# Kernel optimization log

Hardware: AMD Instinct MI355X
Metric: run time of the kernel (lower is better)

The kernel has to match this reference:

```python
import jax, jax.numpy as jnp
import numpy as np

NUM_HEADS = 8
KERNEL = 7  # kernel_size (kh == kw == 7), dilation 1, non-causal


def _na_indices(L, k):
    # NATTEN neighborhood: window start clamped so the kxk window stays in-bounds
    starts = jnp.clip(jnp.arange(L) - k // 2, 0, L - k)  # [L]
    return starts[:, None] + jnp.arange(k)               # [L, k]


def setup_inputs() -> dict:
    key = jax.random.key(0)
    k1, k2, k3 = jax.random.split(key, 3)
    B, H, W, C = 1, 64, 128, 256
    x = jax.random.normal(k1, (B, H, W, C), dtype=jnp.float32)
    # weights stored as [in, out] so y = x @ w + b (equivalent to torch Linear math)
    w_qkv = jax.random.normal(k2, (C, 3 * C), dtype=jnp.float32) * 0.02
    b_qkv = jnp.zeros((3 * C,), dtype=jnp.float32)
    w_proj = jax.random.normal(k3, (C, C), dtype=jnp.float32) * 0.02
    b_proj = jnp.zeros((C,), dtype=jnp.float32)
    return {"x": x, "w_qkv": w_qkv, "b_qkv": b_qkv, "w_proj": w_proj, "b_proj": b_proj}


def reference(x, w_qkv, b_qkv, w_proj, b_proj):
    B, H, W, C = x.shape
    nh = NUM_HEADS
    hd = C // nh
    scale = hd ** -0.5
    kk = KERNEL

    qkv = (x @ w_qkv + b_qkv).reshape(B, H, W, 3, nh, hd)
    q = qkv[:, :, :, 0]  # [B,H,W,nh,hd]
    k = qkv[:, :, :, 1]
    v = qkv[:, :, :, 2]

    ih = _na_indices(H, kk)  # [H,kk]
    iw = _na_indices(W, kk)  # [W,kk]

    # gather K/V neighborhoods: [B,H,kh,W,kw,nh,hd]
    k_win = k[:, ih][:, :, :, iw]
    v_win = v[:, ih][:, :, :, iw]

    # scores: query vs its kh*kw neighbors
    attn = jnp.einsum('bhwnd,bhpwqnd->bhwnpq', q * scale, k_win)  # [B,H,W,nh,kh,kw]
    attn = jax.nn.softmax(attn.reshape(B, H, W, nh, kk * kk), axis=-1)
    attn = attn.reshape(B, H, W, nh, kk, kk)

    out = jnp.einsum('bhwnpq,bhpwqnd->bhwnd', attn, v_win)  # [B,H,W,nh,hd]
    out = out.reshape(B, H, W, C)
    return out @ w_proj + b_proj
```

## Files before the change

kernel.cpp:

```cpp
#include <hip/hip_runtime.h>
#include <cmath>

#define HH 64
#define WW 128
#define CC 256
#define NHEAD 8
#define HDIM 32
#define NPIX (HH*WW)
#define QKV_N (3*CC)

#define KSLOT 248
#define LDK   40
#define VSLOT 264

typedef __attribute__((ext_vector_type(8))) short short8v;
typedef __attribute__((ext_vector_type(4))) short short4v;
typedef __attribute__((ext_vector_type(4))) float f32x4;
typedef unsigned int u32;

__device__ __forceinline__ short f2bf(float f) {
    unsigned int u = __builtin_bit_cast(unsigned int, f);
    u += 0x7fffu + ((u >> 16) & 1u);
    return (short)(u >> 16);
}

__global__ __launch_bounds__(256)
void prep_w(const float* __restrict__ w_qkv, const float* __restrict__ w_proj,
            short* __restrict__ wq_t, short* __restrict__ wp_t)
{
    __shared__ float tile[32][33];
    int idx = blockIdx.x;
    const float* src; short* dst; int N;
    if (idx < 192) { src = w_qkv;  dst = wq_t; N = QKV_N; }
    else { idx -= 192; src = w_proj; dst = wp_t; N = CC; }
    const int nbx = N / 32;
    const int bn = (idx % nbx) * 32;
    const int bk = (idx / nbx) * 32;
    const int tx = threadIdx.x & 31, ty = threadIdx.x >> 5;
#pragma unroll
    for (int i = 0; i < 32; i += 8)
        tile[ty + i][tx] = src[(size_t)(bk + ty + i) * N + bn + tx];
    __syncthreads();
#pragma unroll
    for (int i = 0; i < 32; i += 8)
        dst[(size_t)(bn + ty + i) * CC + bk + tx] = f2bf(tile[tx][ty + i]);
}

__global__ __launch_bounds__(256)
void gemm_qkv(const float* __restrict__ A, const short* __restrict__ Bt,
              const float* __restrict__ bias, short* __restrict__ Cp)
{
    __shared__ short As[64 * 40];
    __shared__ short Bs[2][128 * 32];

    const int tid = threadIdx.x, lane = tid & 63, wave = tid >> 6;
    const int wm0 = (wave >> 1) * 32, wn0 = (wave & 1) * 64;
    const int bm = blockIdx.x * 64, bn = blockIdx.y * 128;
    const int l15 = lane & 15, l4 = lane >> 4;
    const int arow = tid >> 2, akoff = (tid & 3) * 8;

    f32x4 acc[2][4];
#pragma unroll
    for (int i = 0; i < 2; ++i)
#pragma unroll
        for (int j = 0; j < 4; ++j) acc[i][j] = (f32x4){0.f, 0.f, 0.f, 0.f};

    auto stageB = [&](int buf, int t) {
#pragma unroll
        for (int i = 0; i < 2; ++i) {
            const int g = tid + 256 * i;
            const int row = g >> 2, gr = g & 3;
            __builtin_amdgcn_global_load_lds(
                (const __attribute__((address_space(1))) u32*)
                    (Bt + (size_t)(bn + row) * CC + t * 32 + ((gr ^ (row & 3)) * 8)),
                (__attribute__((address_space(3))) u32*)&Bs[buf][g * 8], 16, 0, 0);
        }
    };

    float4 a0, a1;
    {
        const float* p = A + (size_t)(bm + arow) * CC + akoff;
        a0 = *(const float4*)p; a1 = *(const float4*)(p + 4);
    }
    stageB(0, 0);

    for (int t = 0; t < 8; ++t) {
        const int cur = t & 1;
        __syncthreads();
        {
            short8v w;
            w[0] = f2bf(a0.x); w[1] = f2bf(a0.y); w[2] = f2bf(a0.z); w[3] = f2bf(a0.w);
            w[4] = f2bf(a1.x); w[5] = f2bf(a1.y); w[6] = f2bf(a1.z); w[7] = f2bf(a1.w);
            *(short8v*)&As[arow * 40 + akoff] = w;
        }
        __syncthreads();
        if (t + 1 < 8) {
            const float* p = A + (size_t)(bm + arow) * CC + (t + 1) * 32 + akoff;
            a0 = *(const float4*)p; a1 = *(const float4*)(p + 4);
            stageB(cur ^ 1, t + 1);
        }

        short8v af[2], bf[4];
#pragma unroll
        for (int fm = 0; fm < 2; ++fm)
            af[fm] = *(const short8v*)&As[(wm0 + fm * 16 + l15) * 40 + l4 * 8];
#pragma unroll
        for (int fn = 0; fn < 4; ++fn) {
            const int row = wn0 + fn * 16 + l15;
            bf[fn] = *(const short8v*)&Bs[cur][row * 32 + ((l4 ^ (row & 3)) * 8)];
        }
#pragma unroll
        for (int fm = 0; fm < 2; ++fm)
#pragma unroll
            for (int fn = 0; fn < 4; ++fn)
                acc[fm][fn] = __builtin_amdgcn_mfma_f32_16x16x32_bf16(
                    af[fm], bf[fn], acc[fm][fn], 0, 0, 0);
    }

    const int col0 = bn + wn0 + l15;
    const int row0 = bm + wm0 + l4 * 4;
#pragma unroll
    for (int fn = 0; fn < 4; ++fn) {
        const int cc = col0 + fn * 16;
        const float bv = bias[cc];
#pragma unroll
        for (int fm = 0; fm < 2; ++fm)
#pragma unroll
            for (int r = 0; r < 4; ++r) {
                const int rr = row0 + fm * 16 + r;
                Cp[((size_t)(cc >> 5) * NPIX + rr) * HDIM + (cc & 31)] =
                    f2bf(acc[fm][fn][r] + bv);
            }
    }
}

__global__ __launch_bounds__(256)
void gemm_proj(const short* __restrict__ A, const short* __restrict__ Bt,
               const float* __restrict__ bias, float* __restrict__ C)
{
    __shared__ short As[2][64 * 32];
    __shared__ short Bs[2][128 * 32];

    const int tid = threadIdx.x, lane = tid & 63, wave = tid >> 6;
    const int wm0 = (wave >> 1) * 32, wn0 = (wave & 1) * 64;
    const int bm = blockIdx.x * 64, bn = blockIdx.y * 128;
    const int l15 = lane & 15, l4 = lane >> 4;

    f32x4 acc[2][4];
#pragma unroll
    for (int i = 0; i < 2; ++i)
#pragma unroll
        for (int j = 0; j < 4; ++j) acc[i][j] = (f32x4){0.f, 0.f, 0.f, 0.f};

    auto stage = [&](int buf, int t) {
        {
            const int row = tid >> 2, gr = tid & 3;
            __builtin_amdgcn_global_load_lds(
                (const __attribute__((address_space(1))) u32*)
                    (A + (size_t)(bm + row) * CC + t * 32 + ((gr ^ (row & 3)) * 8)),
                (__attribute__((address_space(3))) u32*)&As[buf][tid * 8], 16, 0, 0);
        }
#pragma unroll
        for (int i = 0; i < 2; ++i) {
            const int g = tid + 256 * i;
            const int row = g >> 2, gr = g & 3;
            __builtin_amdgcn_global_load_lds(
                (const __attribute__((address_space(1))) u32*)
                    (Bt + (size_t)(bn + row) * CC + t * 32 + ((gr ^ (row & 3)) * 8)),
                (__attribute__((address_space(3))) u32*)&Bs[buf][g * 8], 16, 0, 0);
        }
    };

    stage(0, 0);

    for (int t = 0; t < 8; ++t) {
        const int cur = t & 1;
        __syncthreads();
        if (t + 1 < 8) stage(cur ^ 1, t + 1);

        short8v af[2], bf[4];
#pragma unroll
        for (int fm = 0; fm < 2; ++fm) {
            const int row = wm0 + fm * 16 + l15;
            af[fm] = *(const short8v*)&As[cur][row * 32 + ((l4 ^ (row & 3)) * 8)];
        }
#pragma unroll
        for (int fn = 0; fn < 4; ++fn) {
            const int row = wn0 + fn * 16 + l15;
            bf[fn] = *(const short8v*)&Bs[cur][row * 32 + ((l4 ^ (row & 3)) * 8)];
        }
#pragma unroll
        for (int fm = 0; fm < 2; ++fm)
#pragma unroll
            for (int fn = 0; fn < 4; ++fn)
                acc[fm][fn] = __builtin_amdgcn_mfma_f32_16x16x32_bf16(
                    af[fm], bf[fn], acc[fm][fn], 0, 0, 0);
    }

    const int col0 = bn + wn0 + l15;
    const int row0 = bm + wm0 + l4 * 4;
#pragma unroll
    for (int fn = 0; fn < 4; ++fn) {
        const float bv = bias[col0 + fn * 16];
#pragma unroll
        for (int fm = 0; fm < 2; ++fm)
#pragma unroll
            for (int r = 0; r < 4; ++r)
                C[(size_t)(row0 + fm * 16 + r) * CC + col0 + fn * 16] =
                    acc[fm][fn][r] + bv;
    }
}

__global__ __launch_bounds__(256)
void na_mfma(const short* __restrict__ qkv, short* __restrict__ attn)
{
    __shared__ short Ksh[KSLOT * LDK];
    __shared__ short Vsh[32 * VSLOT];

    const int x0 = blockIdx.x * 16;
    const int y0 = blockIdx.y * 4;
    const int head = blockIdx.z;
    const int tid = threadIdx.x, lane = tid & 63, w = tid >> 6;
    const int rs  = min(max(y0 - 3, 0), HH - 7);
    const int wsx = x0 - 3;
    const short* Qp = qkv + (size_t)head * NPIX * HDIM;
    const short* Kp = qkv + (size_t)(NHEAD + head) * NPIX * HDIM;
    const short* Vp = qkv + (size_t)(2 * NHEAD + head) * NPIX * HDIM;

    for (int idx = tid; idx < 880; idx += 256) {
        int g = idx & 3, rc = idx >> 2;
        int i = rc / 22, c = rc - i * 22;
        int yy = rs + i, xx = wsx + c;
        if (yy < HH && (unsigned)xx < WW)
            *(short8v*)&Ksh[(i * 24 + c) * LDK + g * 8] =
                *(const short8v*)(Kp + (size_t)(yy * WW + xx) * HDIM + g * 8);
    }
    for (int idx = tid; idx < 264; idx += 256) {
        int g = idx & 3, q2 = idx >> 2;
        int i = q2 / 6, cq = q2 - i * 6;
        int yy = rs + i;
        short8v vv[4];
#pragma unroll
        for (int j = 0; j < 4; ++j) {
            int c = cq * 4 + j, xx = wsx + c;
            if (yy < HH && c < 22 && (unsigned)xx < WW)
                vv[j] = *(const short8v*)(Vp + (size_t)(yy * WW + xx) * HDIM + g * 8);
            else {
                short8v z = {0,0,0,0,0,0,0,0};
                vv[j] = z;
            }
        }
#pragma unroll
        for (int jd = 0; jd < 8; ++jd) {
            short4v s4 = {vv[0][jd], vv[1][jd], vv[2][jd], vv[3][jd]};
            *(short4v*)&Vsh[(g * 8 + jd) * VSLOT + i * 24 + cq * 4] = s4;
        }
    }

    const int l15 = lane & 15, l4 = lane >> 4;
    const int y = y0 + w;
    short8v qf = *(const short8v*)(Qp + (size_t)(y * WW + x0 + l15) * HDIM + l4 * 8);
    __syncthreads();

    const int wbase = (min(max(y - 3, 0), HH - 7) - rs) * 24;

    f32x4 sacc[11];
#pragma unroll
    for (int kc = 0; kc < 11; ++kc) {
        short8v kf = *(const short8v*)&Ksh[(wbase + kc * 16 + l15) * LDK + l4 * 8];
        f32x4 z = {0.f, 0.f, 0.f, 0.f};
        sacc[kc] = __builtin_amdgcn_mfma_f32_16x16x32_bf16(kf, qf, z, 0, 0, 0);
    }

    const int xq = x0 + l15;
    const int cw = min(max(xq - 3, 0), WW - 7) - wsx;
    const float scale = 0.17677669529663687f;
    float lsum = 0.f;
#pragma unroll
    for (int kc = 0; kc < 11; ++kc) {
#pragma unroll
        for (int r = 0; r < 4; ++r) {
            int kl = kc * 16 + l4 * 4 + r;
            int row = kl / 24;
            int c = kl - row * 24;
            bool valid = (row < 7) && (c >= cw) && (c <= cw + 6);
            float e = valid ? __expf(sacc[kc][r] * scale) : 0.f;
            sacc[kc][r] = e;
            lsum += e;
        }
    }
    lsum += __shfl_xor(lsum, 16);
    lsum += __shfl_xor(lsum, 32);
    const float inv = 1.0f / lsum;

    short4v pf[12];
#pragma unroll
    for (int kc = 0; kc < 11; ++kc) {
        short4v pk;
#pragma unroll
        for (int r = 0; r < 4; ++r) pk[r] = f2bf(sacc[kc][r] * inv);
        pf[kc] = pk;
    }
    pf[11] = (short4v){0, 0, 0, 0};

    const int src0 = ((l4 & 1) << 5) + l15;
    const int src1 = src0 + 16;
    const bool hi = (l4 & 2) != 0;
    f32x4 oacc[2];
    oacc[0] = (f32x4){0.f, 0.f, 0.f, 0.f};
    oacc[1] = (f32x4){0.f, 0.f, 0.f, 0.f};
#pragma unroll
    for (int kc2 = 0; kc2 < 6; ++kc2) {
        int lo0 = ((const int*)&pf[2 * kc2])[0];
        int lo1 = ((const int*)&pf[2 * kc2])[1];
        int hi0 = ((const int*)&pf[2 * kc2 + 1])[0];
        int hi1 = ((const int*)&pf[2 * kc2 + 1])[1];
        int a0 = __shfl(lo0, src0), a1 = __shfl(lo1, src0);
        int a2 = __shfl(lo0, src1), a3 = __shfl(lo1, src1);
        int b0 = __shfl(hi0, src0), b1 = __shfl(hi1, src0);
        int b2 = __shfl(hi0, src1), b3 = __shfl(hi1, src1);
        int w0 = hi ? b0 : a0, w1 = hi ? b1 : a1;
        int w2 = hi ? b2 : a2, w3 = hi ? b3 : a3;
        int wv[4] = {w0, w1, w2, w3};
        short8v bfrag = *(const short8v*)wv;
#pragma unroll
        for (int nc = 0; nc < 2; ++nc) {
            short8v vf = *(const short8v*)&Vsh[(nc * 16 + l15) * VSLOT
                                               + wbase + kc2 * 32 + l4 * 8];
            oacc[nc] = __builtin_amdgcn_mfma_f32_16x16x32_bf16(vf, bfrag, oacc[nc], 0, 0, 0);
        }
    }

    short* op = attn + (size_t)(y * WW + x0 + l15) * CC + head * HDIM;
#pragma unroll
    for (int nc = 0; nc < 2; ++nc) {
        short4v o;
#pragma unroll
        for (int r = 0; r < 4; ++r) o[r] = f2bf(oacc[nc][r]);
        *(short4v*)(op + nc * 16 + l4 * 4) = o;
    }
}

extern "C" void kernel_launch(void* const* d_in, const int* in_sizes, int n_in,
                              void* d_out, int out_size, void* d_ws, size_t ws_size,
                              hipStream_t stream)
{
    const float* x      = (const float*)d_in[0];
    const float* w_qkv  = (const float*)d_in[1];
    const float* b_qkv  = (const float*)d_in[2];
    const float* w_proj = (const float*)d_in[3];
    const float* b_proj = (const float*)d_in[4];
    float* out = (float*)d_out;

    char* ws = (char*)d_ws;
    short* qkv_r   = (short*)ws;
    short* attn_bf = (short*)(ws + 12582912);
    short* wq_t    = (short*)(ws + 16777216);
    short* wp_t    = (short*)(ws + 17170432);

    prep_w<<<dim3(256), dim3(256), 0, stream>>>(w_qkv, w_proj, wq_t, wp_t);

    gemm_qkv<<<dim3(NPIX / 64, QKV_N / 128), dim3(256), 0, stream>>>(
        x, wq_t, b_qkv, qkv_r);

    na_mfma<<<dim3(WW / 16, HH / 4, NHEAD), dim3(256), 0, stream>>>(qkv_r, attn_bf);

    gemm_proj<<<dim3(NPIX / 64, CC / 128), dim3(256), 0, stream>>>(
        attn_bf, wp_t, b_proj, out);
}
```

Baseline: 43.89 us.

## Fuse four stages into one persistent kernel with hierarchical grid barriers

```diff
diff --git a/kernel.cpp b/kernel.cpp
--- a/kernel.cpp
+++ b/kernel.cpp
@@ -8,6 +8,7 @@
 #define HDIM 32
 #define NPIX (HH*WW)
 #define QKV_N (3*CC)
+#define NBLK 1024u
 
 #define KSLOT 248
 #define LDK   40
@@ -24,12 +25,39 @@
     return (short)(u >> 16);
 }
 
-__global__ __launch_bounds__(256)
-void prep_w(const float* __restrict__ w_qkv, const float* __restrict__ w_proj,
-            short* __restrict__ wq_t, short* __restrict__ wp_t)
-{
-    __shared__ float tile[32][33];
-    int idx = blockIdx.x;
+__device__ __forceinline__ void grid_sync(u32* syncb, u32 bar, int bid)
+{
+    __syncthreads();
+    if (threadIdx.x == 0) {
+        u32* sub   = syncb + (bid & 7) * 32;
+        u32* top   = syncb + 8 * 32;
+        u32* flagv = syncb + (9 + (bid & 7)) * 32;
+        u32 prev = __hip_atomic_fetch_add(sub, 1u, __ATOMIC_ACQ_REL,
+                                          __HIP_MEMORY_SCOPE_AGENT);
+        if (prev == bar * (NBLK / 8u) - 1u) {
+            u32 p2 = __hip_atomic_fetch_add(top, 1u, __ATOMIC_ACQ_REL,
+                                            __HIP_MEMORY_SCOPE_AGENT);
+            if (p2 == bar * 8u - 1u) {
+#pragma unroll
+                for (int r = 0; r < 8; ++r)
+                    __hip_atomic_store(syncb + (9 + r) * 32, bar,
+                                       __ATOMIC_RELEASE, __HIP_MEMORY_SCOPE_AGENT);
+            }
+        }
+        while (__hip_atomic_fetch_add(flagv, 0u, __ATOMIC_RELAXED,
+                                      __HIP_MEMORY_SCOPE_AGENT) < bar)
+            __builtin_amdgcn_s_sleep(32);
+        (void)__hip_atomic_load(flagv, __ATOMIC_ACQUIRE,
+                                __HIP_MEMORY_SCOPE_AGENT);
+    }
+    __syncthreads();
+}
+
+__device__ __forceinline__ void prep_unit(float* ldsf, int idx,
+    const float* __restrict__ w_qkv, const float* __restrict__ w_proj,
+    short* __restrict__ wq_t, short* __restrict__ wp_t)
+{
+    float (*tile)[33] = reinterpret_cast<float(*)[33]>(ldsf);
     const float* src; short* dst; int N;
     if (idx < 192) { src = w_qkv;  dst = wq_t; N = QKV_N; }
     else { idx -= 192; src = w_proj; dst = wp_t; N = CC; }
@@ -46,16 +74,15 @@
         dst[(size_t)(bn + ty + i) * CC + bk + tx] = f2bf(tile[tx][ty + i]);
 }
 
-__global__ __launch_bounds__(256)
-void gemm_qkv(const float* __restrict__ A, const short* __restrict__ Bt,
-              const float* __restrict__ bias, short* __restrict__ Cp)
-{
-    __shared__ short As[64 * 40];
-    __shared__ short Bs[2][128 * 32];
+__device__ __forceinline__ void qkv_tile(short* lds,
+    const float* __restrict__ A, const short* __restrict__ Bt,
+    const float* __restrict__ bias, short* __restrict__ Cp, int bm, int bn)
+{
+    short* As = lds;
+    short* Bs = lds + 64 * 40;
 
     const int tid = threadIdx.x, lane = tid & 63, wave = tid >> 6;
     const int wm0 = (wave >> 1) * 32, wn0 = (wave & 1) * 64;
-    const int bm = blockIdx.x * 64, bn = blockIdx.y * 128;
     const int l15 = lane & 15, l4 = lane >> 4;
     const int arow = tid >> 2, akoff = (tid & 3) * 8;
 
@@ -73,7 +100,8 @@
             __builtin_amdgcn_global_load_lds(
                 (const __attribute__((address_space(1))) u32*)
                     (Bt + (size_t)(bn + row) * CC + t * 32 + ((gr ^ (row & 3)) * 8)),
-                (__attribute__((address_space(3))) u32*)&Bs[buf][g * 8], 16, 0, 0);
+                (__attribute__((address_space(3))) u32*)&Bs[buf * 128 * 32 + g * 8],
+                16, 0, 0);
         }
     };
 
@@ -107,7 +135,7 @@
 #pragma unroll
         for (int fn = 0; fn < 4; ++fn) {
             const int row = wn0 + fn * 16 + l15;
-            bf[fn] = *(const short8v*)&Bs[cur][row * 32 + ((l4 ^ (row & 3)) * 8)];
+            bf[fn] = *(const short8v*)&Bs[cur * 128 * 32 + row * 32 + ((l4 ^ (row & 3)) * 8)];
         }
 #pragma unroll
         for (int fm = 0; fm < 2; ++fm)
@@ -134,16 +162,15 @@
     }
 }
 
-__global__ __launch_bounds__(256)
-void gemm_proj(const short* __restrict__ A, const short* __restrict__ Bt,
-               const float* __restrict__ bias, float* __restrict__ C)
-{
-    __shared__ short As[2][64 * 32];
-    __shared__ short Bs[2][128 * 32];
+__device__ __forceinline__ void proj_tile(short* lds,
+    const short* __restrict__ A, const short* __restrict__ Bt,
+    const float* __restrict__ bias, float* __restrict__ C, int bm, int bn)
+{
+    short* As = lds;
+    short* Bs = lds + 2 * 64 * 32;
 
     const int tid = threadIdx.x, lane = tid & 63, wave = tid >> 6;
     const int wm0 = (wave >> 1) * 32, wn0 = (wave & 1) * 64;
-    const int bm = blockIdx.x * 64, bn = blockIdx.y * 128;
     const int l15 = lane & 15, l4 = lane >> 4;
 
     f32x4 acc[2][4];
@@ -158,7 +185,8 @@
             __builtin_amdgcn_global_load_lds(
                 (const __attribute__((address_space(1))) u32*)
                     (A + (size_t)(bm + row) * CC + t * 32 + ((gr ^ (row & 3)) * 8)),
-                (__attribute__((address_space(3))) u32*)&As[buf][tid * 8], 16, 0, 0);
+                (__attribute__((address_space(3))) u32*)&As[buf * 64 * 32 + tid * 8],
+                16, 0, 0);
         }
 #pragma unroll
         for (int i = 0; i < 2; ++i) {
@@ -167,7 +195,8 @@
             __builtin_amdgcn_global_load_lds(
                 (const __attribute__((address_space(1))) u32*)
                     (Bt + (size_t)(bn + row) * CC + t * 32 + ((gr ^ (row & 3)) * 8)),
-                (__attribute__((address_space(3))) u32*)&Bs[buf][g * 8], 16, 0, 0);
+                (__attribute__((address_space(3))) u32*)&Bs[buf * 128 * 32 + g * 8],
+                16, 0, 0);
         }
     };
 
@@ -182,12 +211,12 @@
 #pragma unroll
         for (int fm = 0; fm < 2; ++fm) {
             const int row = wm0 + fm * 16 + l15;
-            af[fm] = *(const short8v*)&As[cur][row * 32 + ((l4 ^ (row & 3)) * 8)];
+            af[fm] = *(const short8v*)&As[cur * 64 * 32 + row * 32 + ((l4 ^ (row & 3)) * 8)];
         }
 #pragma unroll
         for (int fn = 0; fn < 4; ++fn) {
             const int row = wn0 + fn * 16 + l15;
-            bf[fn] = *(const short8v*)&Bs[cur][row * 32 + ((l4 ^ (row & 3)) * 8)];
+            bf[fn] = *(const short8v*)&Bs[cur * 128 * 32 + row * 32 + ((l4 ^ (row & 3)) * 8)];
         }
 #pragma unroll
         for (int fm = 0; fm < 2; ++fm)
@@ -211,15 +240,13 @@
     }
 }
 
-__global__ __launch_bounds__(256)
-void na_mfma(const short* __restrict__ qkv, short* __restrict__ attn)
-{
-    __shared__ short Ksh[KSLOT * LDK];
-    __shared__ short Vsh[32 * VSLOT];
-
-    const int x0 = blockIdx.x * 16;
-    const int y0 = blockIdx.y * 4;
-    const int head = blockIdx.z;
+__device__ __forceinline__ void na_tile(short* lds, const short* __restrict__ qkv,
+                                        short* __restrict__ attn,
+                                        int x0, int y0, int head)
+{
+    short* Ksh = lds;
+    short* Vsh = lds + KSLOT * LDK;
+
     const int tid = threadIdx.x, lane = tid & 63, w = tid >> 6;
     const int rs  = min(max(y0 - 3, 0), HH - 7);
     const int wsx = x0 - 3;
@@ -341,6 +368,32 @@
     }
 }
 
+__global__ __launch_bounds__(256, 4)
+void fused(const float* __restrict__ x, const float* __restrict__ w_qkv,
+           const float* __restrict__ b_qkv, const float* __restrict__ w_proj,
+           const float* __restrict__ b_proj, float* __restrict__ out,
+           short* __restrict__ wq_t, short* __restrict__ wp_t,
+           short* __restrict__ qkv_r, short* __restrict__ attn_bf, u32* syncb)
+{
+    __shared__ f32x4 shq[2296];
+    short* sh = (short*)shq;
+    const int bid = blockIdx.x;
+
+    if (bid < 256)
+        prep_unit((float*)shq, bid, w_qkv, w_proj, wq_t, wp_t);
+    grid_sync(syncb, 1, bid);
+
+    if (bid < 768)
+        qkv_tile(sh, x, wq_t, b_qkv, qkv_r, (bid & 127) * 64, (bid >> 7) * 128);
+    grid_sync(syncb, 2, bid);
+
+    na_tile(sh, qkv_r, attn_bf, (bid & 7) * 16, ((bid >> 3) & 15) * 4, bid >> 7);
+    grid_sync(syncb, 3, bid);
+
+    if (bid < 256)
+        proj_tile(sh, attn_bf, wp_t, b_proj, out, (bid & 127) * 64, (bid >> 7) * 128);
+}
+
 extern "C" void kernel_launch(void* const* d_in, const int* in_sizes, int n_in,
                               void* d_out, int out_size, void* d_ws, size_t ws_size,
                               hipStream_t stream)
@@ -357,14 +410,10 @@
     short* attn_bf = (short*)(ws + 12582912);
     short* wq_t    = (short*)(ws + 16777216);
     short* wp_t    = (short*)(ws + 17170432);
-
-    prep_w<<<dim3(256), dim3(256), 0, stream>>>(w_qkv, w_proj, wq_t, wp_t);
-
-    gemm_qkv<<<dim3(NPIX / 64, QKV_N / 128), dim3(256), 0, stream>>>(
-        x, wq_t, b_qkv, qkv_r);
-
-    na_mfma<<<dim3(WW / 16, HH / 4, NHEAD), dim3(256), 0, stream>>>(qkv_r, attn_bf);
-
-    gemm_proj<<<dim3(NPIX / 64, CC / 128), dim3(256), 0, stream>>>(
-        attn_bf, wp_t, b_proj, out);
-}
+    u32*   syncb   = (u32*)(ws + 17301504);
+
+    hipMemsetAsync(syncb, 0, 2176, stream);
+    fused<<<dim3(NBLK), dim3(256), 0, stream>>>(
+        x, w_qkv, b_qkv, w_proj, b_proj, out,
+        wq_t, wp_t, qkv_r, attn_bf, syncb);
+}
```

After: 174.5 us. 298% more time.

## Drop weight prep kernel; load fp32 weights into registers in GEMMs

Applied to the files above, without the earlier changes.

```diff
diff --git a/kernel.cpp b/kernel.cpp
--- a/kernel.cpp
+++ b/kernel.cpp
@@ -25,106 +25,65 @@
 }
 
 __global__ __launch_bounds__(256)
-void prep_w(const float* __restrict__ w_qkv, const float* __restrict__ w_proj,
-            short* __restrict__ wq_t, short* __restrict__ wp_t)
-{
-    __shared__ float tile[32][33];
-    int idx = blockIdx.x;
-    const float* src; short* dst; int N;
-    if (idx < 192) { src = w_qkv;  dst = wq_t; N = QKV_N; }
-    else { idx -= 192; src = w_proj; dst = wp_t; N = CC; }
-    const int nbx = N / 32;
-    const int bn = (idx % nbx) * 32;
-    const int bk = (idx / nbx) * 32;
-    const int tx = threadIdx.x & 31, ty = threadIdx.x >> 5;
-#pragma unroll
-    for (int i = 0; i < 32; i += 8)
-        tile[ty + i][tx] = src[(size_t)(bk + ty + i) * N + bn + tx];
-    __syncthreads();
-#pragma unroll
-    for (int i = 0; i < 32; i += 8)
-        dst[(size_t)(bn + ty + i) * CC + bk + tx] = f2bf(tile[tx][ty + i]);
-}
-
-__global__ __launch_bounds__(256)
-void gemm_qkv(const float* __restrict__ A, const short* __restrict__ Bt,
+void gemm_qkv(const float* __restrict__ A, const float* __restrict__ W,
               const float* __restrict__ bias, short* __restrict__ Cp)
 {
-    __shared__ short As[64 * 40];
-    __shared__ short Bs[2][128 * 32];
-
     const int tid = threadIdx.x, lane = tid & 63, wave = tid >> 6;
-    const int wm0 = (wave >> 1) * 32, wn0 = (wave & 1) * 64;
-    const int bm = blockIdx.x * 64, bn = blockIdx.y * 128;
+    const int bm = blockIdx.x * 128, bn = blockIdx.y * 64;
+    const int wm0 = (wave >> 1) * 64, wn0 = (wave & 1) * 32;
     const int l15 = lane & 15, l4 = lane >> 4;
-    const int arow = tid >> 2, akoff = (tid & 3) * 8;
-
-    f32x4 acc[2][4];
-#pragma unroll
-    for (int i = 0; i < 2; ++i)
-#pragma unroll
-        for (int j = 0; j < 4; ++j) acc[i][j] = (f32x4){0.f, 0.f, 0.f, 0.f};
-
-    auto stageB = [&](int buf, int t) {
-#pragma unroll
-        for (int i = 0; i < 2; ++i) {
-            const int g = tid + 256 * i;
-            const int row = g >> 2, gr = g & 3;
-            __builtin_amdgcn_global_load_lds(
-                (const __attribute__((address_space(1))) u32*)
-                    (Bt + (size_t)(bn + row) * CC + t * 32 + ((gr ^ (row & 3)) * 8)),
-                (__attribute__((address_space(3))) u32*)&Bs[buf][g * 8], 16, 0, 0);
-        }
-    };
-
-    float4 a0, a1;
-    {
-        const float* p = A + (size_t)(bm + arow) * CC + akoff;
-        a0 = *(const float4*)p; a1 = *(const float4*)(p + 4);
-    }
-    stageB(0, 0);
-
+
+    short8v bbr[2][8];
+#pragma unroll
+    for (int fn = 0; fn < 2; ++fn) {
+        const int n = bn + wn0 + fn * 16 + l15;
+#pragma unroll
+        for (int t = 0; t < 8; ++t) {
+            const float* wp = W + (size_t)(t * 32 + l4 * 8) * QKV_N + n;
+            short8v b;
+#pragma unroll
+            for (int j = 0; j < 8; ++j)
+                b[j] = f2bf(wp[(size_t)j * QKV_N]);
+            bbr[fn][t] = b;
+        }
+    }
+
+    f32x4 acc[4][2];
+#pragma unroll
+    for (int i = 0; i < 4; ++i)
+#pragma unroll
+        for (int j = 0; j < 2; ++j) acc[i][j] = (f32x4){0.f, 0.f, 0.f, 0.f};
+
+#pragma unroll
     for (int t = 0; t < 8; ++t) {
-        const int cur = t & 1;
-        __syncthreads();
-        {
+        short8v af[4];
+#pragma unroll
+        for (int fm = 0; fm < 4; ++fm) {
+            const float* p = A + (size_t)(bm + wm0 + fm * 16 + l15) * CC
+                             + t * 32 + l4 * 8;
+            float4 a0 = *(const float4*)p;
+            float4 a1 = *(const float4*)(p + 4);
             short8v w;
             w[0] = f2bf(a0.x); w[1] = f2bf(a0.y); w[2] = f2bf(a0.z); w[3] = f2bf(a0.w);
             w[4] = f2bf(a1.x); w[5] = f2bf(a1.y); w[6] = f2bf(a1.z); w[7] = f2bf(a1.w);
-            *(short8v*)&As[arow * 40 + akoff] = w;
-        }
-        __syncthreads();
-        if (t + 1 < 8) {
-            const float* p = A + (size_t)(bm + arow) * CC + (t + 1) * 32 + akoff;
-            a0 = *(const float4*)p; a1 = *(const float4*)(p + 4);
-            stageB(cur ^ 1, t + 1);
-        }
-
-        short8v af[2], bf[4];
-#pragma unroll
-        for (int fm = 0; fm < 2; ++fm)
-            af[fm] = *(const short8v*)&As[(wm0 + fm * 16 + l15) * 40 + l4 * 8];
-#pragma unroll
-        for (int fn = 0; fn < 4; ++fn) {
-            const int row = wn0 + fn * 16 + l15;
-            bf[fn] = *(const short8v*)&Bs[cur][row * 32 + ((l4 ^ (row & 3)) * 8)];
-        }
-#pragma unroll
-        for (int fm = 0; fm < 2; ++fm)
-#pragma unroll
-            for (int fn = 0; fn < 4; ++fn)
+            af[fm] = w;
+        }
+#pragma unroll
+        for (int fm = 0; fm < 4; ++fm)
+#pragma unroll
+            for (int fn = 0; fn < 2; ++fn)
                 acc[fm][fn] = __builtin_amdgcn_mfma_f32_16x16x32_bf16(
-                    af[fm], bf[fn], acc[fm][fn], 0, 0, 0);
+                    af[fm], bbr[fn][t], acc[fm][fn], 0, 0, 0);
     }
 
     const int col0 = bn + wn0 + l15;
     const int row0 = bm + wm0 + l4 * 4;
 #pragma unroll
-    for (int fn = 0; fn < 4; ++fn) {
+    for (int fn = 0; fn < 2; ++fn) {
         const int cc = col0 + fn * 16;
         const float bv = bias[cc];
 #pragma unroll
-        for (int fm = 0; fm < 2; ++fm)
+        for (int fm = 0; fm < 4; ++fm)
 #pragma unroll
             for (int r = 0; r < 4; ++r) {
                 const int rr = row0 + fm * 16 + r;
@@ -135,72 +94,54 @@
 }
 
 __global__ __launch_bounds__(256)
-void gemm_proj(const short* __restrict__ A, const short* __restrict__ Bt,
+void gemm_proj(const short* __restrict__ A, const float* __restrict__ W,
                const float* __restrict__ bias, float* __restrict__ C)
 {
-    __shared__ short As[2][64 * 32];
-    __shared__ short Bs[2][128 * 32];
-
     const int tid = threadIdx.x, lane = tid & 63, wave = tid >> 6;
-    const int wm0 = (wave >> 1) * 32, wn0 = (wave & 1) * 64;
-    const int bm = blockIdx.x * 64, bn = blockIdx.y * 128;
+    const int bm = blockIdx.x * 64, bn = blockIdx.y * 64;
+    const int wm0 = (wave >> 1) * 32, wn0 = (wave & 1) * 32;
     const int l15 = lane & 15, l4 = lane >> 4;
 
-    f32x4 acc[2][4];
+    short8v bbr[2][8];
+#pragma unroll
+    for (int fn = 0; fn < 2; ++fn) {
+        const int n = bn + wn0 + fn * 16 + l15;
+#pragma unroll
+        for (int t = 0; t < 8; ++t) {
+            const float* wp = W + (size_t)(t * 32 + l4 * 8) * CC + n;
+            short8v b;
+#pragma unroll
+            for (int j = 0; j < 8; ++j)
+                b[j] = f2bf(wp[(size_t)j * CC]);
+            bbr[fn][t] = b;
+        }
+    }
+
+    f32x4 acc[2][2];
 #pragma unroll
     for (int i = 0; i < 2; ++i)
 #pragma unroll
-        for (int j = 0; j < 4; ++j) acc[i][j] = (f32x4){0.f, 0.f, 0.f, 0.f};
-
-    auto stage = [&](int buf, int t) {
-        {
-            const int row = tid >> 2, gr = tid & 3;
-            __builtin_amdgcn_global_load_lds(
-                (const __attribute__((address_space(1))) u32*)
-                    (A + (size_t)(bm + row) * CC + t * 32 + ((gr ^ (row & 3)) * 8)),
-                (__attribute__((address_space(3))) u32*)&As[buf][tid * 8], 16, 0, 0);
-        }
-#pragma unroll
-        for (int i = 0; i < 2; ++i) {
-            const int g = tid + 256 * i;
-            const int row = g >> 2, gr = g & 3;
-            __builtin_amdgcn_global_load_lds(
-                (const __attribute__((address_space(1))) u32*)
-                    (Bt + (size_t)(bn + row) * CC + t * 32 + ((gr ^ (row & 3)) * 8)),
-                (__attribute__((address_space(3))) u32*)&Bs[buf][g * 8], 16, 0, 0);
-        }
-    };
-
-    stage(0, 0);
-
+        for (int j = 0; j < 2; ++j) acc[i][j] = (f32x4){0.f, 0.f, 0.f, 0.f};
+
+#pragma unroll
     for (int t = 0; t < 8; ++t) {
-        const int cur = t & 1;
-        __syncthreads();
-        if (t + 1 < 8) stage(cur ^ 1, t + 1);
-
-        short8v af[2], bf[4];
-#pragma unroll
-        for (int fm = 0; fm < 2; ++fm) {
-            const int row = wm0 + fm * 16 + l15;
-            af[fm] = *(const short8v*)&As[cur][row * 32 + ((l4 ^ (row & 3)) * 8)];
-        }
-#pragma unroll
-        for (int fn = 0; fn < 4; ++fn) {
-            const int row = wn0 + fn * 16 + l15;
-            bf[fn] = *(const short8v*)&Bs[cur][row * 32 + ((l4 ^ (row & 3)) * 8)];
-        }
+        short8v af[2];
 #pragma unroll
         for (int fm = 0; fm < 2; ++fm)
-#pragma unroll
-            for (int fn = 0; fn < 4; ++fn)
+            af[fm] = *(const short8v*)(A + (size_t)(bm + wm0 + fm * 16 + l15) * CC
+                                       + t * 32 + l4 * 8);
+#pragma unroll
+        for (int fm = 0; fm < 2; ++fm)
+#pragma unroll
+            for (int fn = 0; fn < 2; ++fn)
                 acc[fm][fn] = __builtin_amdgcn_mfma_f32_16x16x32_bf16(
-                    af[fm], bf[fn], acc[fm][fn], 0, 0, 0);
+                    af[fm], bbr[fn][t], acc[fm][fn], 0, 0, 0);
     }
 
     const int col0 = bn + wn0 + l15;
     const int row0 = bm + wm0 + l4 * 4;
 #pragma unroll
-    for (int fn = 0; fn < 4; ++fn) {
+    for (int fn = 0; fn < 2; ++fn) {
         const float bv = bias[col0 + fn * 16];
 #pragma unroll
         for (int fm = 0; fm < 2; ++fm)
@@ -355,16 +296,12 @@
     char* ws = (char*)d_ws;
     short* qkv_r   = (short*)ws;
     short* attn_bf = (short*)(ws + 12582912);
-    short* wq_t    = (short*)(ws + 16777216);
-    short* wp_t    = (short*)(ws + 17170432);
-
-    prep_w<<<dim3(256), dim3(256), 0, stream>>>(w_qkv, w_proj, wq_t, wp_t);
-
-    gemm_qkv<<<dim3(NPIX / 64, QKV_N / 128), dim3(256), 0, stream>>>(
-        x, wq_t, b_qkv, qkv_r);
+
+    gemm_qkv<<<dim3(NPIX / 128, QKV_N / 64), dim3(256), 0, stream>>>(
+        x, w_qkv, b_qkv, qkv_r);
 
     na_mfma<<<dim3(WW / 16, HH / 4, NHEAD), dim3(256), 0, stream>>>(qkv_r, attn_bf);
 
-    gemm_proj<<<dim3(NPIX / 64, CC / 128), dim3(256), 0, stream>>>(
-        attn_bf, wp_t, b_proj, out);
-}
+    gemm_proj<<<dim3(NPIX / 64, CC / 64), dim3(256), 0, stream>>>(
+        attn_bf, w_proj, b_proj, out);
+}
```

Result: slower. 56.40 us (+28.5%).
